# Optimization experiments

Hardware: AMD Instinct MI355X
Metric: run time of the kernel (lower is better)

Reference implementation:

```python
import jax, jax.numpy as jnp
import numpy as np
from jax import lax

B, N, D = 8, 4096, 768
H, K, U, V = 12, 16, 4, 64   # heads, key_depth, intra_depth, lambda_query_size
L = 23                        # local_context_size (odd)
PAD = L // 2
EPS = 1e-5


def setup_inputs() -> dict:
    key = jax.random.key(0)
    ks = jax.random.split(key, 9)
    return {
        "x": jax.random.normal(ks[0], (B, N, D), dtype=jnp.float32),
        "Wq": jax.random.normal(ks[1], (H * K, D), dtype=jnp.float32) * 0.02,
        "Wk": jax.random.normal(ks[2], (K * U, D), dtype=jnp.float32) * 0.02,
        "Wv": jax.random.normal(ks[3], (V * U, D), dtype=jnp.float32) * 0.02,
        "gamma_q": 1.0 + 0.1 * jax.random.normal(ks[4], (H * K,), dtype=jnp.float32),
        "beta_q": 0.1 * jax.random.normal(ks[5], (H * K,), dtype=jnp.float32),
        "gamma_v": 1.0 + 0.1 * jax.random.normal(ks[6], (V * U,), dtype=jnp.float32),
        "beta_v": 0.1 * jax.random.normal(ks[7], (V * U,), dtype=jnp.float32),
        "rel_pos_embed": jax.random.normal(ks[8], (K, U, 1, L), dtype=jnp.float32),
    }


def _batchnorm1d(z, gamma, beta):
    # z: (b, c, n); training-mode BatchNorm1d (biased variance over batch+length)
    mean = jnp.mean(z, axis=(0, 2), keepdims=True)
    var = jnp.mean((z - mean) ** 2, axis=(0, 2), keepdims=True)
    zhat = (z - mean) * lax.rsqrt(var + EPS)
    return zhat * gamma[None, :, None] + beta[None, :, None]


def reference(x, Wq, Wk, Wv, gamma_q, beta_q, gamma_v, beta_v, rel_pos_embed):
    b, n, d = x.shape
    xT = jnp.swapaxes(x, 1, 2)                      # b d n
    q = jnp.einsum('od,bdn->bon', Wq, xT)           # b (h k) n
    k = jnp.einsum('od,bdn->bon', Wk, xT)           # b (k u) n
    v = jnp.einsum('od,bdn->bon', Wv, xT)           # b (v u) n
    q = _batchnorm1d(q, gamma_q, beta_q)
    v = _batchnorm1d(v, gamma_v, beta_v)
    q = q.reshape(b, H, K, n)                       # b h k n
    k = k.reshape(b, K, U, n).transpose(0, 2, 1, 3) # b u k n
    v = v.reshape(b, V, U, n).transpose(0, 2, 1, 3) # b u v n
    k = jax.nn.softmax(k, axis=-1)                  # softmax over positions
    lam_c = jnp.einsum('bukn,buvn->bkv', k, v)      # content lambda
    Yc = jnp.einsum('bhkn,bkv->bnhv', q, lam_c)
    # position lambda via local conv over positions: v (b,u,V,n) * W (K,u,1,L) -> (b,K,V,n)
    lam_p = lax.conv_general_dilated(
        v, rel_pos_embed, window_strides=(1, 1),
        padding=((0, 0), (PAD, PAD)),
        dimension_numbers=('NCHW', 'OIHW', 'NCHW'))
    Yp = jnp.einsum('bhkn,bkvn->bnhv', q, lam_p)
    Y = (Yc + Yp).reshape(b, n, H * V)
    return Y
```

## Files before the change

### kernel.cpp

```cpp
#include <hip/hip_runtime.h>
#include <hip/hip_bf16.h>

constexpr int B = 8, N = 4096, D = 768;
constexpr int H = 12, K = 16, U = 4, V = 64, L = 23, PAD = 11;
constexpr int CQ = 192;
constexpr int CK = 64;
constexpr int CV = 256;
constexpr int CT = 512;
constexpr int CV0 = CQ + CK;
constexpr float EPS = 1e-5f;

typedef _Float16 f16x8 __attribute__((ext_vector_type(8)));
typedef _Float16 f16x4 __attribute__((ext_vector_type(4)));
typedef _Float16 f16x2 __attribute__((ext_vector_type(2)));
typedef float    f32x4 __attribute__((ext_vector_type(4)));

#define GLOAD16(gp, lp) __builtin_amdgcn_global_load_lds( \
    (const __attribute__((address_space(1))) void*)(gp),  \
    (__attribute__((address_space(3))) void*)(lp), 16, 0, 0)

__device__ __forceinline__ f16x2 pkrtz(float a, float b) {
    return __builtin_bit_cast(f16x2, __builtin_amdgcn_cvt_pkrtz(a, b));
}

__device__ __forceinline__ f16x8 cvt8r(float4 a, float4 b) {
    f16x8 r;
    r[0] = (_Float16)a.x; r[1] = (_Float16)a.y; r[2] = (_Float16)a.z; r[3] = (_Float16)a.w;
    r[4] = (_Float16)b.x; r[5] = (_Float16)b.y; r[6] = (_Float16)b.z; r[7] = (_Float16)b.w;
    return r;
}

__global__ __launch_bounds__(256) void k_w16(
    const float* __restrict__ Wq, const float* __restrict__ Wk,
    const float* __restrict__ Wv, const float* __restrict__ rel,
    _Float16* __restrict__ Wh, _Float16* __restrict__ relSg)
{
    const int bid = blockIdx.x;
    const int tid = threadIdx.x;
    if (bid < 192) {
        const int idx = bid * 256 + tid;
        const int c = idx / 96, g = idx % 96;
        const float* src;
        if (c < CQ)       src = Wq + (size_t)c * D;
        else if (c < CV0) src = Wk + (size_t)(c - CQ) * D;
        else              src = Wv + (size_t)(c - CV0) * D;
        float4 a = *(const float4*)(src + g * 8);
        float4 b = *(const float4*)(src + g * 8 + 4);
        *(f16x8*)(Wh + (size_t)c * D + g * 8) = cvt8r(a, b);
    } else {
        const int base = ((bid - 192) * 256 + tid) * 8;
        f16x8 o;
        #pragma unroll
        for (int j = 0; j < 8; ++j) {
            const int e = base + j;
            const int jj = e & 31, kk = (e >> 5) & 15;
            const int uu = (e >> 9) & 3, dd = e >> 11;
            const int l = jj - dd;
            float v = (l >= 0 && l < L) ? rel[(kk * U + uu) * L + l] : 0.f;
            o[j] = (_Float16)v;
        }
        *(f16x8*)(relSg + base) = o;
    }
}

__global__ __launch_bounds__(512) void k_proj(
    const float* __restrict__ x, const _Float16* __restrict__ Wh,
    _Float16* __restrict__ Ph)
{
    __shared__ _Float16 As0[512 * 32], As1[512 * 32], As2[512 * 32];
    __shared__ float    Bs0[128 * 32], Bs1[128 * 32], Bs2[128 * 32];
    const int b  = blockIdx.z;
    const int bn = blockIdx.x * 128;
    const int tid  = threadIdx.x;
    const int lane = tid & 63;
    const int wave = tid >> 6;
    const int wr  = wave >> 1;
    const int wcn = wave & 1;
    const int fr = lane & 15, sl = lane >> 4;

    const int arow_l = lane >> 2;
    const int achk   = (lane & 3) ^ (arow_l & 3) ^ ((arow_l >> 2) & 3);
    const int brow_l = lane >> 3;
    const int bchk   = (lane & 7) ^ brow_l;

    const _Float16* Wbase = Wh;
    const float*    xbase = x + ((size_t)b * N + bn) * D;

    const int ca = sl ^ (fr & 3) ^ ((fr >> 2) & 3);
    const int mb = fr & 7;

    f32x4 acc[8][4] = {};

#define STAGE(Ap, Bp, kt) do {                                         \
        _Pragma("unroll")                                              \
        for (int j = 0; j < 4; ++j) {                                  \
            const int r0 = wave * 64 + j * 16;                         \
            GLOAD16(Wbase + (size_t)(r0 + arow_l) * D + (kt) + achk * 8, \
                    (Ap) + r0 * 32);                                   \
        }                                                              \
        _Pragma("unroll")                                              \
        for (int j = 0; j < 2; ++j) {                                  \
            const int r0 = wave * 16 + j * 8;                          \
            GLOAD16(xbase + (size_t)(r0 + brow_l) * D + (kt) + bchk * 4, \
                    (Bp) + r0 * 32);                                   \
        }                                                              \
    } while (0)

#define WAIT6  asm volatile("s_waitcnt vmcnt(6)" ::: "memory")
#define WAIT0  asm volatile("s_waitcnt vmcnt(0)" ::: "memory")
#define BAR    __builtin_amdgcn_s_barrier()
#define SCHED0 __builtin_amdgcn_sched_barrier(0)

#define PHASE(Ap, Bp, StageStmt, WaitStmt) do {                        \
        f16x8 af[8]; float4 pa[4], pb[4];                              \
        _Pragma("unroll")                                              \
        for (int mi = 0; mi < 8; ++mi) {                               \
            const int ra = wr * 128 + mi * 16 + fr;                    \
            af[mi] = *(const f16x8*)((Ap) + ra * 32 + ca * 8);         \
        }                                                              \
        _Pragma("unroll")                                              \
        for (int ni = 0; ni < 4; ++ni) {                               \
            const int rb = wcn * 64 + ni * 16 + fr;                    \
            pa[ni] = *(const float4*)((Bp) + rb * 32 + (((sl * 2) ^ mb) * 4)); \
            pb[ni] = *(const float4*)((Bp) + rb * 32 + (((sl * 2 + 1) ^ mb) * 4)); \
        }                                                              \
        StageStmt;                                                     \
        WaitStmt;                                                      \
        SCHED0; BAR;                                                   \
        f16x8 bfr[4];                                                  \
        _Pragma("unroll")                                              \
        for (int ni = 0; ni < 4; ++ni) {                               \
            f16x2 p0 = pkrtz(pa[ni].x, pa[ni].y);                      \
            f16x2 p1 = pkrtz(pa[ni].z, pa[ni].w);                      \
            f16x2 p2 = pkrtz(pb[ni].x, pb[ni].y);                      \
            f16x2 p3 = pkrtz(pb[ni].z, pb[ni].w);                      \
            f16x8 bv;                                                  \
            bv[0] = p0[0]; bv[1] = p0[1]; bv[2] = p1[0]; bv[3] = p1[1]; \
            bv[4] = p2[0]; bv[5] = p2[1]; bv[6] = p3[0]; bv[7] = p3[1]; \
            bfr[ni] = bv;                                              \
        }                                                              \
        __builtin_amdgcn_s_setprio(1);                                 \
        _Pragma("unroll")                                              \
        for (int mi = 0; mi < 8; ++mi)                                 \
            _Pragma("unroll")                                          \
            for (int ni = 0; ni < 4; ++ni)                             \
                acc[mi][ni] = __builtin_amdgcn_mfma_f32_16x16x32_f16(  \
                    af[mi], bfr[ni], acc[mi][ni], 0, 0, 0);            \
        __builtin_amdgcn_s_setprio(0);                                 \
        SCHED0; BAR;                                                   \
    } while (0)

    STAGE(As0, Bs0, 0);
    STAGE(As1, Bs1, 32);
    WAIT6;
    BAR;

    for (int t0 = 0; t0 < 21; t0 += 3) {
        const int kt = t0 * 32;
        PHASE(As0, Bs0, STAGE(As2, Bs2, kt + 64),  WAIT6);
        PHASE(As1, Bs1, STAGE(As0, Bs0, kt + 96),  WAIT6);
        PHASE(As2, Bs2, STAGE(As1, Bs1, kt + 128), WAIT6);
    }
    PHASE(As0, Bs0, STAGE(As2, Bs2, 736), WAIT6);
    PHASE(As1, Bs1, (void)0, WAIT0);
    PHASE(As2, Bs2, (void)0, (void)0);

#undef STAGE
#undef PHASE
#undef WAIT6
#undef WAIT0
#undef BAR
#undef SCHED0

    _Float16* Pb = Ph + (size_t)b * CT * N + bn;
    #pragma unroll
    for (int mi = 0; mi < 8; ++mi)
        #pragma unroll
        for (int ni = 0; ni < 4; ++ni)
            #pragma unroll
            for (int r = 0; r < 4; ++r) {
                const int row = wr * 128 + mi * 16 + sl * 4 + r;
                const int col = wcn * 64 + ni * 16 + fr;
                Pb[(size_t)row * N + col] = (_Float16)acc[mi][ni][r];
            }
}

__global__ __launch_bounds__(256) void k_stats(
    const _Float16* __restrict__ Ph,
    const float* __restrict__ gq, const float* __restrict__ bq,
    const float* __restrict__ gv, const float* __restrict__ bv,
    float* __restrict__ sArr, float* __restrict__ tArr,
    float* __restrict__ mxk, float* __restrict__ invk,
    float* __restrict__ lamC)
{
    const int bid = blockIdx.x;
    const int tid = threadIdx.x;

    if (bid < CQ + CV) {
        const int ci = bid;
        const int c  = (ci < CQ) ? ci : ci + CK;
        float g, be;
        if (ci < CQ) { g = gq[ci];      be = bq[ci]; }
        else         { g = gv[ci - CQ]; be = bv[ci - CQ]; }

        float s = 0.f, s2 = 0.f;
        for (int b = 0; b < B; ++b) {
            const _Float16* row = Ph + ((size_t)b * CT + c) * N;
            #pragma unroll
            for (int i = 0; i < 2; ++i) {
                f16x8 v = ((const f16x8*)row)[i * 256 + tid];
                #pragma unroll
                for (int j = 0; j < 8; ++j) {
                    float f = (float)v[j];
                    s += f; s2 += f * f;
                }
            }
        }
        #pragma unroll
        for (int off = 32; off; off >>= 1) {
            s  += __shfl_xor(s, off);
            s2 += __shfl_xor(s2, off);
        }
        __shared__ float ls[4], ls2[4];
        if ((tid & 63) == 0) { ls[tid >> 6] = s; ls2[tid >> 6] = s2; }
        __syncthreads();
        if (tid == 0) {
            float S = ls[0] + ls[1] + ls[2] + ls[3];
            float S2 = ls2[0] + ls2[1] + ls2[2] + ls2[3];
            const float invM = 1.0f / (float)(B * N);
            float mean = S * invM;
            float var  = S2 * invM - mean * mean;
            float sc   = g / sqrtf(var + EPS);
            sArr[c] = sc;
            tArr[c] = be - mean * sc;
        }
    } else {
        const int idx = bid - (CQ + CV);
        if (idx < 8) {
            ((float4*)lamC)[idx * 256 + tid] = float4{0.f, 0.f, 0.f, 0.f};
        }
        const int b = idx >> 6, kc = idx & 63;
        const _Float16* row = Ph + ((size_t)b * CT + CQ + kc) * N;
        float v[16];
        float m = -3.4e38f;
        #pragma unroll
        for (int i = 0; i < 2; ++i) {
            f16x8 t = ((const f16x8*)row)[i * 256 + tid];
            #pragma unroll
            for (int j = 0; j < 8; ++j) {
                v[i*8+j] = (float)t[j];
                m = fmaxf(m, v[i*8+j]);
            }
        }
        #pragma unroll
        for (int off = 32; off; off >>= 1) m = fmaxf(m, __shfl_xor(m, off));
        __shared__ float rA[4], rB[4];
        if ((tid & 63) == 0) rA[tid >> 6] = m;
        __syncthreads();
        m = fmaxf(fmaxf(rA[0], rA[1]), fmaxf(rA[2], rA[3]));
        float s = 0.f;
        #pragma unroll
        for (int i = 0; i < 16; ++i) s += __expf(v[i] - m);
        #pragma unroll
        for (int off = 32; off; off >>= 1) s += __shfl_xor(s, off);
        if ((tid & 63) == 0) rB[tid >> 6] = s;
        __syncthreads();
        if (tid == 0) {
            s = rB[0] + rB[1] + rB[2] + rB[3];
            mxk[b * CK + kc]  = m;
            invk[b * CK + kc] = 1.f / s;
        }
    }
}

__global__ __launch_bounds__(256) void k_mid(
    const _Float16* __restrict__ Ph, const float* __restrict__ mxk,
    const float* __restrict__ invk, const float* __restrict__ sArr,
    const float* __restrict__ tArr, float* __restrict__ lamC,
    _Float16* __restrict__ qT)
{
    __shared__ float smem[128 * 20 + 128 * 67];
    const int bid = blockIdx.x;
    const int tid = threadIdx.x;

    if (bid < 256) {
        float (*Kt)[20] = (float(*)[20])smem;
        float (*Vt)[67] = (float(*)[67])(smem + 128 * 20);
        const int cx = bid & 7, u = (bid >> 3) & 3, b = bid >> 5;
        const int chunk0 = cx * 512;
        const int vv = tid & 63, kg = tid >> 6;
        float acc[4] = {0.f, 0.f, 0.f, 0.f};

        const int kk = tid >> 4, sK = tid & 15;
        const float mm = mxk[b * CK + kk * U + u];
        const float iv = invk[b * CK + kk * U + u];

        for (int sc = 0; sc < 4; ++sc) {
            const int nbase = chunk0 + sc * 128;
            __syncthreads();
            {
                f16x8 v = *(const f16x8*)(Ph + ((size_t)b * CT + CQ + kk * U + u) * N
                                          + nbase + sK * 8);
                #pragma unroll
                for (int i = 0; i < 8; ++i)
                    Kt[sK * 8 + i][kk] = __expf((float)v[i] - mm) * iv;
            }
            {
                #pragma unroll
                for (int it = 0; it < 4; ++it) {
                    const int task = it * 256 + tid;
                    const int vvv = task >> 4, sV = task & 15;
                    const int c = CV0 + vvv * U + u;
                    f16x8 v = *(const f16x8*)(Ph + ((size_t)b * CT + c) * N
                                              + nbase + sV * 8);
                    const float sc2 = sArr[c], tt = tArr[c];
                    #pragma unroll
                    for (int i = 0; i < 8; ++i)
                        Vt[sV * 8 + i][vvv] = (float)v[i] * sc2 + tt;
                }
            }
            __syncthreads();
            #pragma unroll 4
            for (int n = 0; n < 128; ++n) {
                float4 kv = *(const float4*)&Kt[n][kg * 4];
                float vx = Vt[n][vv];
                acc[0] += kv.x * vx; acc[1] += kv.y * vx;
                acc[2] += kv.z * vx; acc[3] += kv.w * vx;
            }
        }
        #pragma unroll
        for (int j = 0; j < 4; ++j)
            atomicAdd(&lamC[((size_t)b * K + kg * 4 + j) * V + vv], acc[j]);
    } else {
        _Float16 (*tl)[40] = (_Float16(*)[40])smem;
        const int q  = bid - 256;
        const int n0 = (q & 63) * 64;
        const int c0 = ((q >> 6) % 6) * 32;
        const int b  = q / 384;

        const int ch = tid >> 3, seg = tid & 7;
        const int c = c0 + ch;
        f16x8 v = *(const f16x8*)(Ph + ((size_t)b * CT + c) * N + n0 + seg * 8);
        const float sc = sArr[c], tt = tArr[c];
        #pragma unroll
        for (int i = 0; i < 8; ++i)
            tl[seg * 8 + i][ch] = (_Float16)((float)v[i] * sc + tt);
        __syncthreads();

        const int n = tid >> 2, part = tid & 3;
        f16x8 o = *(const f16x8*)&tl[n][part * 8];
        *(f16x8*)(qT + ((size_t)b * N + n0 + n) * CQ + c0 + part * 8) = o;
    }
}

__global__ __launch_bounds__(512, 4) void k_out(
    const _Float16* __restrict__ Ph, const _Float16* __restrict__ relSg,
    const float* __restrict__ lamC, const float* __restrict__ sArr,
    const float* __restrict__ tArr, const _Float16* __restrict__ qT,
    float* __restrict__ Y)
{
    constexpr int NT = 32;
    constexpr int VST = 72;
    __shared__ _Float16 vsegT[256 * VST];

    const int b  = blockIdx.y;
    const int n0 = blockIdx.x * NT;
    const int tid  = threadIdx.x;
    const int lane = tid & 63;
    const int wave = tid >> 6;
    const int fr = lane & 15;
    const int sl = lane >> 4;

    #pragma unroll
    for (int it = 0; it < 4; ++it) {
        const int task = it * 512 + tid;
        const int ch = task >> 3, s = task & 7;
        const int c = CV0 + ch;
        const int row = (ch & 3) * 64 + (ch >> 2);
        const int nbase = n0 - 16 + s * 8;
        const float sc = sArr[c], tt = tArr[c];
        const bool full = (nbase >= 0) && (nbase + 8 <= N);
        f16x8 v{};
        if (full)
            v = *(const f16x8*)(Ph + ((size_t)b * CT + c) * N + nbase);
        #pragma unroll
        for (int i = 0; i < 8; ++i) {
            const int np = s * 8 - 5 + i;
            if (np < 0 || np >= 56) continue;
            float val = 0.f;
            if (full) {
                val = (float)v[i] * sc + tt;
            } else {
                const int n = nbase + i;
                if (n >= 0 && n < N)
                    val = (float)Ph[((size_t)b * CT + c) * N + n] * sc + tt;
            }
            vsegT[row * VST + np] = (_Float16)val;
        }
    }
    const int vg = wave & 3;
    const int nb = (wave >> 2) * 16;
    float lc[4];
    #pragma unroll
    for (int r = 0; r < 4; ++r)
        lc[r] = lamC[(size_t)b * K * V + (sl * 4 + r) * V + vg * 16 + fr];
    __syncthreads();

    const _Float16* qTb = qT + (size_t)b * N * CQ;

    for (int dlt = 0; dlt < 8; ++dlt) {
        f16x8 aU[4];
        #pragma unroll
        for (int u = 0; u < 4; ++u)
            aU[u] = *(const f16x8*)(relSg + ((dlt * 4 + u) * 16 + fr) * 32 + sl * 8);
        #pragma unroll
        for (int rep = 0; rep < 2; ++rep) {
            const int A  = nb + rep * 8;
            const int nn = A + dlt;
            f32x4 acc = {lc[0], lc[1], lc[2], lc[3]};
            #pragma unroll
            for (int u = 0; u < 4; ++u) {
                f16x8 bf = *(const f16x8*)(vsegT + (u * 64 + vg * 16 + fr) * VST + A + sl * 8);
                acc = __builtin_amdgcn_mfma_f32_16x16x32_f16(aU[u], bf, acc, 0, 0, 0);
            }
            f16x4 lam16;
            #pragma unroll
            for (int r = 0; r < 4; ++r) lam16[r] = (_Float16)acc[r];
            f16x4 q4 = *(const f16x4*)(qTb + (size_t)(n0 + nn) * CQ + fr * 16 + sl * 4);
            f32x4 y = {0.f, 0.f, 0.f, 0.f};
            y = __builtin_amdgcn_mfma_f32_16x16x16f16(q4, lam16, y, 0, 0, 0);
            if (sl < 3) {
                float* yr = Y + ((size_t)b * N + n0 + nn) * (H * V) + vg * 16 + fr;
                #pragma unroll
                for (int r = 0; r < 4; ++r)
                    yr[(sl * 4 + r) * 64] = y[r];
            }
        }
    }
}

extern "C" void kernel_launch(void* const* d_in, const int* in_sizes, int n_in,
                              void* d_out, int out_size, void* d_ws, size_t ws_size,
                              hipStream_t stream)
{
    const float* x   = (const float*)d_in[0];
    const float* Wq  = (const float*)d_in[1];
    const float* Wk  = (const float*)d_in[2];
    const float* Wv  = (const float*)d_in[3];
    const float* gq  = (const float*)d_in[4];
    const float* bq  = (const float*)d_in[5];
    const float* gv  = (const float*)d_in[6];
    const float* bv  = (const float*)d_in[7];
    const float* rel = (const float*)d_in[8];
    float* Y = (float*)d_out;

    _Float16* Ph  = (_Float16*)d_ws;
    float* sArr = (float*)(Ph + (size_t)B * CT * N);
    float* tArr = sArr + CT;
    float* lamC = tArr + CT;
    float* mxk  = lamC + (size_t)B * K * V;
    float* invk = mxk + B * CK;
    _Float16* qT = (_Float16*)(invk + B * CK);
    _Float16* Wh = qT + (size_t)B * N * CQ;
    _Float16* relSg = Wh + (size_t)CT * D;

    k_w16  <<<dim3(192 + 8), 256, 0, stream>>>(Wq, Wk, Wv, rel, Wh, relSg);
    k_proj <<<dim3(N / 128, 1, B), 512, 0, stream>>>(x, Wh, Ph);
    k_stats<<<dim3(CQ + CV + B * CK), 256, 0, stream>>>(Ph, gq, bq, gv, bv,
                                                        sArr, tArr, mxk, invk, lamC);
    k_mid  <<<dim3(256 + 3072), 256, 0, stream>>>(Ph, mxk, invk, sArr, tArr, lamC, qT);
    k_out  <<<dim3(N / 32, B), 512, 0, stream>>>(Ph, relSg, lamC, sArr, tArr, qT, Y);
}
```

Measured before the change: 112.6 us.

## Fuse query normalize-transpose into output kernel and split lambda blocks finer

Removes the qT intermediate buffer. k_out now loads the query channels for its 32-position tile straight from the projection buffer, applies the batchnorm scale and shift, and transposes them into shared memory. This saves a global write and re-read of the transposed queries. k_mid becomes only the content-lambda reduction, now split into 512 blocks of 256 positions each, which raises parallelism but doubles the atomic adds. k_out's shared memory grows, the minimum-occupancy hint is dropped, and the query gather from Ph uses short strided rows.

```diff
diff --git a/kernel.cpp b/kernel.cpp
--- a/kernel.cpp
+++ b/kernel.cpp
@@ -276,92 +276,69 @@
 __global__ __launch_bounds__(256) void k_mid(
     const _Float16* __restrict__ Ph, const float* __restrict__ mxk,
     const float* __restrict__ invk, const float* __restrict__ sArr,
-    const float* __restrict__ tArr, float* __restrict__ lamC,
-    _Float16* __restrict__ qT)
-{
-    __shared__ float smem[128 * 20 + 128 * 67];
+    const float* __restrict__ tArr, float* __restrict__ lamC)
+{
+    __shared__ float Kt[128][20];
+    __shared__ float Vt[128][67];
     const int bid = blockIdx.x;
     const int tid = threadIdx.x;
-
-    if (bid < 256) {
-        float (*Kt)[20] = (float(*)[20])smem;
-        float (*Vt)[67] = (float(*)[67])(smem + 128 * 20);
-        const int cx = bid & 7, u = (bid >> 3) & 3, b = bid >> 5;
-        const int chunk0 = cx * 512;
-        const int vv = tid & 63, kg = tid >> 6;
-        float acc[4] = {0.f, 0.f, 0.f, 0.f};
-
-        const int kk = tid >> 4, sK = tid & 15;
-        const float mm = mxk[b * CK + kk * U + u];
-        const float iv = invk[b * CK + kk * U + u];
-
-        for (int sc = 0; sc < 4; ++sc) {
-            const int nbase = chunk0 + sc * 128;
-            __syncthreads();
-            {
-                f16x8 v = *(const f16x8*)(Ph + ((size_t)b * CT + CQ + kk * U + u) * N
-                                          + nbase + sK * 8);
+    const int cx = bid & 15, u = (bid >> 4) & 3, b = bid >> 6;
+    const int chunk0 = cx * 256;
+    const int vv = tid & 63, kg = tid >> 6;
+    float acc[4] = {0.f, 0.f, 0.f, 0.f};
+
+    const int kk = tid >> 4, sK = tid & 15;
+    const float mm = mxk[b * CK + kk * U + u];
+    const float iv = invk[b * CK + kk * U + u];
+
+    for (int sc = 0; sc < 2; ++sc) {
+        const int nbase = chunk0 + sc * 128;
+        __syncthreads();
+        {
+            f16x8 v = *(const f16x8*)(Ph + ((size_t)b * CT + CQ + kk * U + u) * N
+                                      + nbase + sK * 8);
+            #pragma unroll
+            for (int i = 0; i < 8; ++i)
+                Kt[sK * 8 + i][kk] = __expf((float)v[i] - mm) * iv;
+        }
+        {
+            #pragma unroll
+            for (int it = 0; it < 4; ++it) {
+                const int task = it * 256 + tid;
+                const int vvv = task >> 4, sV = task & 15;
+                const int c = CV0 + vvv * U + u;
+                f16x8 v = *(const f16x8*)(Ph + ((size_t)b * CT + c) * N
+                                          + nbase + sV * 8);
+                const float sc2 = sArr[c], tt = tArr[c];
                 #pragma unroll
                 for (int i = 0; i < 8; ++i)
-                    Kt[sK * 8 + i][kk] = __expf((float)v[i] - mm) * iv;
-            }
-            {
-                #pragma unroll
-                for (int it = 0; it < 4; ++it) {
-                    const int task = it * 256 + tid;
-                    const int vvv = task >> 4, sV = task & 15;
-                    const int c = CV0 + vvv * U + u;
-                    f16x8 v = *(const f16x8*)(Ph + ((size_t)b * CT + c) * N
-                                              + nbase + sV * 8);
-                    const float sc2 = sArr[c], tt = tArr[c];
-                    #pragma unroll
-                    for (int i = 0; i < 8; ++i)
-                        Vt[sV * 8 + i][vvv] = (float)v[i] * sc2 + tt;
-                }
-            }
-            __syncthreads();
-            #pragma unroll 4
-            for (int n = 0; n < 128; ++n) {
-                float4 kv = *(const float4*)&Kt[n][kg * 4];
-                float vx = Vt[n][vv];
-                acc[0] += kv.x * vx; acc[1] += kv.y * vx;
-                acc[2] += kv.z * vx; acc[3] += kv.w * vx;
-            }
-        }
-        #pragma unroll
-        for (int j = 0; j < 4; ++j)
-            atomicAdd(&lamC[((size_t)b * K + kg * 4 + j) * V + vv], acc[j]);
-    } else {
-        _Float16 (*tl)[40] = (_Float16(*)[40])smem;
-        const int q  = bid - 256;
-        const int n0 = (q & 63) * 64;
-        const int c0 = ((q >> 6) % 6) * 32;
-        const int b  = q / 384;
-
-        const int ch = tid >> 3, seg = tid & 7;
-        const int c = c0 + ch;
-        f16x8 v = *(const f16x8*)(Ph + ((size_t)b * CT + c) * N + n0 + seg * 8);
-        const float sc = sArr[c], tt = tArr[c];
-        #pragma unroll
-        for (int i = 0; i < 8; ++i)
-            tl[seg * 8 + i][ch] = (_Float16)((float)v[i] * sc + tt);
+                    Vt[sV * 8 + i][vvv] = (float)v[i] * sc2 + tt;
+            }
+        }
         __syncthreads();
-
-        const int n = tid >> 2, part = tid & 3;
-        f16x8 o = *(const f16x8*)&tl[n][part * 8];
-        *(f16x8*)(qT + ((size_t)b * N + n0 + n) * CQ + c0 + part * 8) = o;
-    }
-}
-
-__global__ __launch_bounds__(512, 4) void k_out(
+        #pragma unroll 4
+        for (int n = 0; n < 128; ++n) {
+            float4 kv = *(const float4*)&Kt[n][kg * 4];
+            float vx = Vt[n][vv];
+            acc[0] += kv.x * vx; acc[1] += kv.y * vx;
+            acc[2] += kv.z * vx; acc[3] += kv.w * vx;
+        }
+    }
+    #pragma unroll
+    for (int j = 0; j < 4; ++j)
+        atomicAdd(&lamC[((size_t)b * K + kg * 4 + j) * V + vv], acc[j]);
+}
+
+__global__ __launch_bounds__(512) void k_out(
     const _Float16* __restrict__ Ph, const _Float16* __restrict__ relSg,
     const float* __restrict__ lamC, const float* __restrict__ sArr,
-    const float* __restrict__ tArr, const _Float16* __restrict__ qT,
-    float* __restrict__ Y)
+    const float* __restrict__ tArr, float* __restrict__ Y)
 {
     constexpr int NT = 32;
     constexpr int VST = 72;
+    constexpr int QST = 196;
     __shared__ _Float16 vsegT[256 * VST];
+    __shared__ _Float16 qtile[NT * QST];
 
     const int b  = blockIdx.y;
     const int n0 = blockIdx.x * NT;
@@ -398,6 +375,14 @@
             vsegT[row * VST + np] = (_Float16)val;
         }
     }
+    for (int task = tid; task < CQ * 4; task += 512) {
+        const int ch = task >> 2, s = task & 3;
+        f16x8 v = *(const f16x8*)(Ph + ((size_t)b * CT + ch) * N + n0 + s * 8);
+        const float sc = sArr[ch], tt = tArr[ch];
+        #pragma unroll
+        for (int i = 0; i < 8; ++i)
+            qtile[(s * 8 + i) * QST + ch] = (_Float16)((float)v[i] * sc + tt);
+    }
     const int vg = wave & 3;
     const int nb = (wave >> 2) * 16;
     float lc[4];
@@ -406,8 +391,6 @@
         lc[r] = lamC[(size_t)b * K * V + (sl * 4 + r) * V + vg * 16 + fr];
     __syncthreads();
 
-    const _Float16* qTb = qT + (size_t)b * N * CQ;
-
     for (int dlt = 0; dlt < 8; ++dlt) {
         f16x8 aU[4];
         #pragma unroll
@@ -426,7 +409,7 @@
             f16x4 lam16;
             #pragma unroll
             for (int r = 0; r < 4; ++r) lam16[r] = (_Float16)acc[r];
-            f16x4 q4 = *(const f16x4*)(qTb + (size_t)(n0 + nn) * CQ + fr * 16 + sl * 4);
+            f16x4 q4 = *(const f16x4*)(qtile + nn * QST + fr * 16 + sl * 4);
             f32x4 y = {0.f, 0.f, 0.f, 0.f};
             y = __builtin_amdgcn_mfma_f32_16x16x16f16(q4, lam16, y, 0, 0, 0);
             if (sl < 3) {
@@ -460,14 +443,13 @@
     float* lamC = tArr + CT;
     float* mxk  = lamC + (size_t)B * K * V;
     float* invk = mxk + B * CK;
-    _Float16* qT = (_Float16*)(invk + B * CK);
-    _Float16* Wh = qT + (size_t)B * N * CQ;
+    _Float16* Wh = (_Float16*)(invk + B * CK);
     _Float16* relSg = Wh + (size_t)CT * D;
 
     k_w16  <<<dim3(192 + 8), 256, 0, stream>>>(Wq, Wk, Wv, rel, Wh, relSg);
     k_proj <<<dim3(N / 128, 1, B), 512, 0, stream>>>(x, Wh, Ph);
     k_stats<<<dim3(CQ + CV + B * CK), 256, 0, stream>>>(Ph, gq, bq, gv, bv,
                                                         sArr, tArr, mxk, invk, lamC);
-    k_mid  <<<dim3(256 + 3072), 256, 0, stream>>>(Ph, mxk, invk, sArr, tArr, lamC, qT);
-    k_out  <<<dim3(N / 32, B), 512, 0, stream>>>(Ph, relSg, lamC, sArr, tArr, qT, Y);
-}
+    k_mid  <<<dim3(512), 256, 0, stream>>>(Ph, mxk, invk, sArr, tArr, lamC);
+    k_out  <<<dim3(N / 32, B), 512, 0, stream>>>(Ph, relSg, lamC, sArr, tArr, Y);
+}
```

After: 107.1 us (median of 3 runs). 1.05x faster.
